# Optimization experiments

Hardware: AMD Instinct MI355X
Metric: run time of the kernel (lower is better)

The kernel has to match this reference:

```python
import jax, jax.numpy as jnp
import numpy as np

CONT_FIELD = 13
CATE_FIELD = 26
VOCAB = 100000
EMB_DIM = 64
HIDDEN = [1024, 1024]
B = 16384
N_FIELDS = CONT_FIELD + CATE_FIELD            # 39
COMB = N_FIELDS * (N_FIELDS - 1) // 2         # 741
FIRST = EMB_DIM * N_FIELDS + COMB             # 3237

# upper-triangular pair indices (i < j), matching the module's rows/cols
_ROWS, _COLS = np.triu_indices(N_FIELDS, k=1)
ROWS = jnp.asarray(_ROWS)
COLS = jnp.asarray(_COLS)


def setup_inputs() -> dict:
    key = jax.random.key(0)
    ks = jax.random.split(key, 12)
    a = np.square(3.0 / (CATE_FIELD * EMB_DIM))
    inp = {
        "conts": jax.random.uniform(ks[0], (B, CONT_FIELD), dtype=jnp.float32),
        "cates": jax.random.randint(ks[1], (B, CATE_FIELD), 0, VOCAB),
        "combs": jax.random.normal(ks[2], (B, COMB), dtype=jnp.float32),
        "emb_table": jax.random.uniform(ks[3], (VOCAB, EMB_DIM), minval=-a, maxval=a, dtype=jnp.float32),
        "W1": jax.random.normal(ks[4], (FIRST, HIDDEN[0]), dtype=jnp.float32) * (6.0 / (FIRST + HIDDEN[0])) ** 0.5,
        "b1": jnp.zeros((HIDDEN[0],), jnp.float32),
        "ln1_g": jnp.ones((HIDDEN[0],), jnp.float32),
        "ln1_b": jnp.zeros((HIDDEN[0],), jnp.float32),
        "W2": jax.random.normal(ks[5], (HIDDEN[0], HIDDEN[1]), dtype=jnp.float32) * (6.0 / (HIDDEN[0] + HIDDEN[1])) ** 0.5,
        "b2": jnp.zeros((HIDDEN[1],), jnp.float32),
        "ln2_g": jnp.ones((HIDDEN[1],), jnp.float32),
        "ln2_b": jnp.zeros((HIDDEN[1],), jnp.float32),
        "Wout": jax.random.normal(ks[6], (HIDDEN[1], 1), dtype=jnp.float32) * (6.0 / (HIDDEN[1] + 1)) ** 0.5,
        "bout": jnp.zeros((1,), jnp.float32),
    }
    return inp


def _layernorm(x, g, b, eps=1e-5):
    mu = jnp.mean(x, axis=-1, keepdims=True)
    var = jnp.mean((x - mu) ** 2, axis=-1, keepdims=True)
    return (x - mu) * jax.lax.rsqrt(var + eps) * g + b


def reference(conts, cates, combs, emb_table, W1, b1, ln1_g, ln1_b,
              W2, b2, ln2_g, ln2_b, Wout, bout):
    # continuous-field embeddings: rows 0..CONT_FIELD-1 of the table, scaled by values
    cont_emb = emb_table[:CONT_FIELD][None, :, :] * conts[:, :, None]   # [B, 13, D]
    cate_emb = emb_table[cates]                                          # [B, 26, D]
    cc = jnp.concatenate([cont_emb, cate_emb], axis=1)                   # [B, 39, D]
    # pairwise inner products: full Gram then upper-triangle extraction
    gram = jnp.einsum("bfd,bgd->bfg", cc, cc)                            # [B, 39, 39]
    pairs = gram[:, ROWS, COLS]                                          # [B, 741]
    X = jnp.concatenate([cont_emb.reshape(cc.shape[0], -1),
                         cate_emb.reshape(cc.shape[0], -1),
                         pairs], axis=1)                                  # [B, 3237]
    X = jax.nn.relu(_layernorm(X @ W1 + b1, ln1_g, ln1_b))
    X = jax.nn.relu(_layernorm(X @ W2 + b2, ln2_g, ln2_b))
    logit = jax.nn.sigmoid(X @ Wout + bout)                               # [B, 1]
    return logit
```

## Files before the change

### kernel.cpp

```cpp
#include <hip/hip_runtime.h>
#include <hip/hip_bf16.h>

#define BATCH 16384
#define NH 1024
#define NF 39
#define CCLD 72
#define KX 2432
#define NPAIR 741
#define FEAT_BLOCKS (BATCH / 4)
#define WPREP_BX (KX / 32 + NH / 32)
#define WPREP_BLOCKS (WPREP_BX * (NH / 32))

typedef __attribute__((ext_vector_type(8))) short bf16x8;
typedef __attribute__((ext_vector_type(4))) float f32x4;

typedef const __attribute__((address_space(1))) unsigned int* gptr_t;
typedef __attribute__((address_space(3))) unsigned int* lptr_t;

__device__ __forceinline__ float bf2f(unsigned short u) {
  union { unsigned int i; float f; } c; c.i = ((unsigned int)u) << 16; return c.f;
}
__device__ __forceinline__ unsigned short f2bf(float f) {
  union { float f; unsigned int i; } c; c.f = f;
  unsigned int r = c.i + 0x7FFFu + ((c.i >> 16) & 1u);
  return (unsigned short)(r >> 16);
}

__global__ __launch_bounds__(256) void prep_kernel(
    const float* __restrict__ conts, const int* __restrict__ cates,
    const float* __restrict__ emb, unsigned short* __restrict__ X,
    const float* __restrict__ W1, const float* __restrict__ W2,
    unsigned short* __restrict__ W1t, unsigned short* __restrict__ W2t) {
  __shared__ __align__(16) unsigned char smem[33664];

  if (blockIdx.x >= FEAT_BLOCKS) {
    int wq = blockIdx.x - FEAT_BLOCKS;
    int bx = wq % WPREP_BX;
    int nb = (wq / WPREP_BX) * 32;
    float (*tile)[33] = (float(*)[33])smem;
    int tx = threadIdx.x & 31, ty = threadIdx.x >> 5;
    if (bx < KX / 32) {
      int kb = bx * 32;
#pragma unroll
      for (int i = 0; i < 32; i += 8) {
        int k = kb + ty + i;
        float v = 0.f;
        if (k < 13) {
          float s = 0.f;
#pragma unroll 8
          for (int d = 0; d < 64; ++d)
            s += emb[k * 64 + d] * W1[(size_t)(k * 64 + d) * NH + nb + tx];
          v = s;
        } else if (k >= 16 && k < 1680) {
          v = W1[(size_t)(832 + k - 16) * NH + nb + tx];
        } else if (k >= 1680 && k < 1680 + NPAIR) {
          v = W1[(size_t)(2496 + k - 1680) * NH + nb + tx];
        }
        tile[ty + i][tx] = v;
      }
      __syncthreads();
#pragma unroll
      for (int i = 0; i < 32; i += 8)
        W1t[(size_t)(nb + ty + i) * KX + kb + tx] = f2bf(tile[tx][ty + i]);
    } else {
      int kb = (bx - KX / 32) * 32;
#pragma unroll
      for (int i = 0; i < 32; i += 8)
        tile[ty + i][tx] = W2[(size_t)(kb + ty + i) * NH + nb + tx];
      __syncthreads();
#pragma unroll
      for (int i = 0; i < 32; i += 8)
        W2t[(size_t)(nb + ty + i) * NH + kb + tx] = f2bf(tile[tx][ty + i]);
    }
    return;
  }

  int wid = threadIdx.x >> 6, lane = threadIdx.x & 63;
  int b = (blockIdx.x << 2) | wid;
  unsigned short* my = (unsigned short*)smem + wid * (48 * CCLD);
  unsigned short* pw = (unsigned short*)(smem + 27648) + wid * 752;
  unsigned short* Xrow = X + (size_t)b * KX;

  int2 c2[13];
#pragma unroll
  for (int i = 0; i < 13; ++i)
    c2[i] = ((const int2*)(cates + b * 26))[i];
  float cf[13];
#pragma unroll
  for (int f = 0; f < 13; ++f) cf[f] = conts[b * 13 + f];
  float cemb[13];
#pragma unroll
  for (int f = 0; f < 13; ++f) cemb[f] = emb[f * 64 + lane];
  float g[26];
#pragma unroll
  for (int j = 0; j < 26; ++j) {
    int idx = (j & 1) ? c2[j >> 1].y : c2[j >> 1].x;
    g[j] = emb[(size_t)idx * 64 + lane];
  }
#pragma unroll
  for (int f = 0; f < 13; ++f)
    my[f * CCLD + lane] = f2bf(cemb[f] * cf[f]);
#pragma unroll
  for (int j = 0; j < 26; ++j)
    my[(13 + j) * CCLD + lane] = f2bf(g[j]);
#pragma unroll
  for (int f = NF; f < 48; ++f) my[f * CCLD + lane] = 0;
  if (lane < 16) Xrow[lane] = (lane < 13) ? f2bf(cf[lane]) : 0;
  if (lane < 752 - NPAIR) pw[NPAIR + lane] = 0;
  __syncthreads();

#pragma unroll
  for (int i = 0; i < 4; ++i) {
    int q = i * 64 + lane;
    if (q < 208)
      *(bf16x8*)&Xrow[16 + q * 8] =
          *(const bf16x8*)&my[(13 + (q >> 3)) * CCLD + (q & 7) * 8];
  }

  int r15 = lane & 15, hi = lane >> 4;
  bf16x8 fr[2][3];
#pragma unroll
  for (int t = 0; t < 3; ++t)
#pragma unroll
    for (int h = 0; h < 2; ++h)
      fr[h][t] = *(const bf16x8*)&my[(t * 16 + r15) * CCLD + h * 32 + hi * 8];

  f32x4 acc[3][3];
#pragma unroll
  for (int it = 0; it < 3; ++it)
#pragma unroll
    for (int jt = 0; jt < 3; ++jt)
      acc[it][jt] = (f32x4){0.f, 0.f, 0.f, 0.f};
#pragma unroll
  for (int h = 0; h < 2; ++h)
#pragma unroll
    for (int it = 0; it < 3; ++it)
#pragma unroll
      for (int jt = 0; jt < 3; ++jt)
        acc[it][jt] = __builtin_amdgcn_mfma_f32_16x16x32_bf16(
            fr[h][it], fr[h][jt], acc[it][jt], 0, 0, 0);

#pragma unroll
  for (int it = 0; it < 3; ++it)
#pragma unroll
    for (int jt = 0; jt < 3; ++jt) {
      int g_ = jt * 16 + r15;
#pragma unroll
      for (int r = 0; r < 4; ++r) {
        int f = it * 16 + hi * 4 + r;
        if (f < g_ && g_ < NF) {
          int p = f * 38 - ((f * (f - 1)) >> 1) + g_ - f - 1;
          pw[p] = f2bf(acc[it][jt][r]);
        }
      }
    }
  __syncthreads();

#pragma unroll
  for (int i = 0; i < 2; ++i) {
    int q = i * 64 + lane;
    if (q < 94)
      *(bf16x8*)&Xrow[1680 + q * 8] = *(const bf16x8*)&pw[q * 8];
  }
}

#define GLL(s_, d_) __builtin_amdgcn_global_load_lds((gptr_t)(s_), (lptr_t)(d_), 16, 0, 0)
#define RD(p_) (*(const bf16x8*)(p_))
#define DSTA(buf, h) (lds + (buf) * 32768 + (h) * 8192 + sd)
#define DSTB(buf, h) (lds + (buf) * 32768 + 16384 + (h) * 8192 + sd)
#define STG(dst, srcb, tau) do { \
    const unsigned short* _s = (srcb) + (size_t)(tau) * 64; \
    GLL(_s, dst); GLL(_s + (size_t)64 * K, (dst) + 4096); } while (0)
#define FENCE() __builtin_amdgcn_sched_barrier(0)
#define MQ(I0, J0, AB, BB) do { \
    _Pragma("unroll") \
    for (int i_ = 0; i_ < 4; ++i_) \
      _Pragma("unroll") \
      for (int j_ = 0; j_ < 2; ++j_) { \
        acc[(I0) + i_][(J0) + j_] = __builtin_amdgcn_mfma_f32_16x16x32_bf16( \
            AB[i_][0], BB[j_][0], acc[(I0) + i_][(J0) + j_], 0, 0, 0); \
        acc[(I0) + i_][(J0) + j_] = __builtin_amdgcn_mfma_f32_16x16x32_bf16( \
            AB[i_][1], BB[j_][1], acc[(I0) + i_][(J0) + j_], 0, 0, 0); \
      } } while (0)

__global__ __launch_bounds__(512, 2) void gemm_8ph(
    const unsigned short* __restrict__ A, const unsigned short* __restrict__ Bt,
    const float* __restrict__ bias, unsigned short* __restrict__ Hout,
    int K, int NT) {
  __shared__ unsigned short lds[65536];

  int bid = blockIdx.x;
  int swz = (bid & 7) * 32 + (bid >> 3);
  int mb = swz >> 2, nb = swz & 3;
  size_t m0 = (size_t)mb * 256, n0 = (size_t)nb * 256;

  int tid = threadIdx.x, lane = tid & 63, w = tid >> 6;
  int wr = w >> 2, wc = w & 3;
  int r15 = lane & 15, hi = lane >> 4;

  int sr = tid >> 3;
  int ce = ((tid & 7) ^ (sr & 7)) << 3;
  int sd = tid * 8;
  const unsigned short* A0p = A + (m0 + sr) * (size_t)K + ce;
  const unsigned short* A1p = A0p + (size_t)128 * K;
  const unsigned short* B0p = Bt + (n0 + sr) * (size_t)K + ce;
  const unsigned short* B1p = B0p + (size_t)128 * K;

  int cbs = (((hi << 4) ^ ((r15 & 7) << 4)) >> 1);
  int rb0 = r15 * 64 + cbs;
  int rb1 = rb0 ^ 32;
  const unsigned short* aH = lds + wr * 8192;
  const unsigned short* bH = lds + 16384 + (wc >> 1) * 8192 + (wc & 1) * 4096;

  f32x4 acc[8][4];
#pragma unroll
  for (int m = 0; m < 8; ++m)
#pragma unroll
    for (int n = 0; n < 4; ++n) acc[m][n] = (f32x4){0.f, 0.f, 0.f, 0.f};

  bf16x8 a0[4][2], a1[4][2], bS[2][2], bR[2][2];

  {
    int t1 = (NT > 1) ? 1 : 0;
    STG(DSTA(0, 0), A0p, 0);
    STG(DSTA(0, 1), A1p, 0);
    STG(DSTB(0, 0), B0p, 0);
    STG(DSTB(0, 1), B1p, 0);
    STG(DSTA(1, 0), A0p, t1);
    STG(DSTA(1, 1), A1p, t1);
    STG(DSTB(1, 0), B0p, t1);
    STG(DSTB(1, 1), B1p, t1);
    asm volatile("s_waitcnt vmcnt(8)" ::: "memory");
    asm volatile("s_barrier" ::: "memory");
    FENCE();
#pragma unroll
    for (int i = 0; i < 4; ++i) {
      a0[i][0] = RD(aH + i * 1024 + rb0);
      a0[i][1] = RD(aH + i * 1024 + rb1);
    }
  }

  for (int t = 0; t < NT; ++t) {
    int cur = t & 1, nxt = cur ^ 1;
    int tc = (t + 2 < NT) ? t + 2 : NT - 1;
    const unsigned short* aBc = aH + cur * 32768;
    const unsigned short* aBn = aH + nxt * 32768;
    const unsigned short* bB = bH + cur * 32768;

#pragma unroll
    for (int j = 0; j < 2; ++j) {
      bS[j][0] = RD(bB + j * 1024 + rb0);
      bS[j][1] = RD(bB + j * 1024 + rb1);
    }
    asm volatile("s_waitcnt lgkmcnt(0)" ::: "memory");
    FENCE();
    __builtin_amdgcn_s_setprio(1);
    MQ(0, 0, a0, bS);
    __builtin_amdgcn_s_setprio(0);
    FENCE();

#pragma unroll
    for (int j = 0; j < 2; ++j) {
      bR[j][0] = RD(bB + (2 + j) * 1024 + rb0);
      bR[j][1] = RD(bB + (2 + j) * 1024 + rb1);
    }
#pragma unroll
    for (int i = 0; i < 4; ++i) {
      a1[i][0] = RD(aBc + (4 + i) * 1024 + rb0);
      a1[i][1] = RD(aBc + (4 + i) * 1024 + rb1);
    }
    asm volatile("s_waitcnt lgkmcnt(8)" ::: "memory");
    FENCE();
    __builtin_amdgcn_s_setprio(1);
    MQ(0, 2, a0, bR);
    __builtin_amdgcn_s_setprio(0);
    asm volatile("s_waitcnt lgkmcnt(0)" ::: "memory");
    asm volatile("s_barrier" ::: "memory");
    FENCE();

    STG(DSTB(cur, 0), B0p, tc);
    STG(DSTA(cur, 0), A0p, tc);
    STG(DSTA(cur, 1), A1p, tc);
    __builtin_amdgcn_s_setprio(1);
    MQ(4, 2, a1, bR);
    __builtin_amdgcn_s_setprio(0);
    FENCE();

    STG(DSTB(cur, 1), B1p, tc);
    asm volatile("s_waitcnt vmcnt(8)" ::: "memory");
    asm volatile("s_barrier" ::: "memory");
    FENCE();
#pragma unroll
    for (int i = 0; i < 4; ++i) {
      a0[i][0] = RD(aBn + i * 1024 + rb0);
      a0[i][1] = RD(aBn + i * 1024 + rb1);
    }
    FENCE();
    __builtin_amdgcn_s_setprio(1);
    MQ(4, 0, a1, bS);
    __builtin_amdgcn_s_setprio(0);
    FENCE();
  }

  size_t crow = m0 + (size_t)wr * 128 + hi * 4;
  size_t ccol = n0 + (size_t)wc * 64 + r15;
  unsigned short* Hp = Hout + crow * NH + ccol;
  float bv[4];
#pragma unroll
  for (int n = 0; n < 4; ++n) bv[n] = bias[ccol + n * 16];
#pragma unroll
  for (int m = 0; m < 8; ++m)
#pragma unroll
    for (int n = 0; n < 4; ++n)
#pragma unroll
      for (int q = 0; q < 4; ++q)
        Hp[(size_t)(m * 16 + q) * NH + n * 16] = f2bf(acc[m][n][q] + bv[n]);
}

__global__ __launch_bounds__(256) void ln_relu_kernel(
    const unsigned short* __restrict__ Yb, const float* __restrict__ gamma,
    const float* __restrict__ beta, unsigned short* __restrict__ H) {
  int wid = threadIdx.x >> 6, lane = threadIdx.x & 63;
  int b = (blockIdx.x << 2) | wid;
  const unsigned short* yrow = Yb + (size_t)b * NH + lane * 16;
  bf16x8 u0 = *(const bf16x8*)&yrow[0];
  bf16x8 u1 = *(const bf16x8*)&yrow[8];
  float v[16];
#pragma unroll
  for (int i = 0; i < 8; ++i) {
    v[i] = bf2f((unsigned short)u0[i]);
    v[8 + i] = bf2f((unsigned short)u1[i]);
  }
  float s1 = 0.f, s2 = 0.f;
#pragma unroll
  for (int i = 0; i < 16; ++i) { s1 += v[i]; s2 += v[i] * v[i]; }
#pragma unroll
  for (int i = 1; i < 64; i <<= 1) {
    s1 += __shfl_xor(s1, i);
    s2 += __shfl_xor(s2, i);
  }
  float mu = s1 * (1.0f / NH);
  float var = s2 * (1.0f / NH) - mu * mu;
  float rs = rsqrtf(var + 1e-5f);
  const float4* gp = (const float4*)(gamma + lane * 16);
  const float4* bp = (const float4*)(beta + lane * 16);
  unsigned short o[16];
#pragma unroll
  for (int q = 0; q < 4; ++q) {
    float4 gg = gp[q], be = bp[q];
    o[q * 4 + 0] = f2bf(fmaxf((v[q * 4 + 0] - mu) * rs * gg.x + be.x, 0.f));
    o[q * 4 + 1] = f2bf(fmaxf((v[q * 4 + 1] - mu) * rs * gg.y + be.y, 0.f));
    o[q * 4 + 2] = f2bf(fmaxf((v[q * 4 + 2] - mu) * rs * gg.z + be.z, 0.f));
    o[q * 4 + 3] = f2bf(fmaxf((v[q * 4 + 3] - mu) * rs * gg.w + be.w, 0.f));
  }
  unsigned short* hrow = H + (size_t)b * NH + lane * 16;
  *(ulonglong2*)&hrow[0] = *(const ulonglong2*)&o[0];
  *(ulonglong2*)&hrow[8] = *(const ulonglong2*)&o[8];
}

__global__ __launch_bounds__(256) void ln_out_kernel(
    const unsigned short* __restrict__ Yb, const float* __restrict__ gamma,
    const float* __restrict__ beta, const float* __restrict__ Wout,
    const float* __restrict__ bout, float* __restrict__ out) {
  int wid = threadIdx.x >> 6, lane = threadIdx.x & 63;
  int b = (blockIdx.x << 2) | wid;
  const unsigned short* yrow = Yb + (size_t)b * NH + lane * 16;
  bf16x8 u0 = *(const bf16x8*)&yrow[0];
  bf16x8 u1 = *(const bf16x8*)&yrow[8];
  float v[16];
#pragma unroll
  for (int i = 0; i < 8; ++i) {
    v[i] = bf2f((unsigned short)u0[i]);
    v[8 + i] = bf2f((unsigned short)u1[i]);
  }
  float s1 = 0.f, s2 = 0.f;
#pragma unroll
  for (int i = 0; i < 16; ++i) { s1 += v[i]; s2 += v[i] * v[i]; }
#pragma unroll
  for (int i = 1; i < 64; i <<= 1) {
    s1 += __shfl_xor(s1, i);
    s2 += __shfl_xor(s2, i);
  }
  float mu = s1 * (1.0f / NH);
  float var = s2 * (1.0f / NH) - mu * mu;
  float rs = rsqrtf(var + 1e-5f);
  const float4* gp = (const float4*)(gamma + lane * 16);
  const float4* bp = (const float4*)(beta + lane * 16);
  const float4* wp = (const float4*)(Wout + lane * 16);
  float s = 0.f;
#pragma unroll
  for (int q = 0; q < 4; ++q) {
    float4 gg = gp[q], be = bp[q], wo = wp[q];
    s += fmaxf((v[q * 4 + 0] - mu) * rs * gg.x + be.x, 0.f) * wo.x;
    s += fmaxf((v[q * 4 + 1] - mu) * rs * gg.y + be.y, 0.f) * wo.y;
    s += fmaxf((v[q * 4 + 2] - mu) * rs * gg.z + be.z, 0.f) * wo.z;
    s += fmaxf((v[q * 4 + 3] - mu) * rs * gg.w + be.w, 0.f) * wo.w;
  }
#pragma unroll
  for (int i = 1; i < 64; i <<= 1) s += __shfl_xor(s, i);
  if (lane == 0) out[b] = 1.f / (1.f + expf(-(s + bout[0])));
}

extern "C" void kernel_launch(void* const* d_in, const int* in_sizes, int n_in,
                              void* d_out, int out_size, void* d_ws, size_t ws_size,
                              hipStream_t stream) {
  const float* conts = (const float*)d_in[0];
  const int* cates = (const int*)d_in[1];
  const float* emb  = (const float*)d_in[3];
  const float* W1   = (const float*)d_in[4];
  const float* b1   = (const float*)d_in[5];
  const float* ln1g = (const float*)d_in[6];
  const float* ln1b = (const float*)d_in[7];
  const float* W2   = (const float*)d_in[8];
  const float* b2   = (const float*)d_in[9];
  const float* ln2g = (const float*)d_in[10];
  const float* ln2b = (const float*)d_in[11];
  const float* Wout = (const float*)d_in[12];
  const float* bout = (const float*)d_in[13];
  float* out = (float*)d_out;

  unsigned short* X   = (unsigned short*)d_ws;
  unsigned short* W1t = X + (size_t)BATCH * KX;
  unsigned short* W2t = W1t + (size_t)NH * KX;
  unsigned short* H1  = W2t + (size_t)NH * NH;
  unsigned short* Yb1 = H1 + (size_t)BATCH * NH;
  unsigned short* Yb2 = Yb1 + (size_t)BATCH * NH;

  hipLaunchKernelGGL(prep_kernel, dim3(FEAT_BLOCKS + WPREP_BLOCKS), dim3(256), 0, stream,
                     conts, cates, emb, X, W1, W2, W1t, W2t);
  hipLaunchKernelGGL(gemm_8ph, dim3(256), dim3(512), 0, stream,
                     X, W1t, b1, Yb1, KX, KX / 64);
  hipLaunchKernelGGL(ln_relu_kernel, dim3(BATCH / 4), dim3(256), 0, stream,
                     Yb1, ln1g, ln1b, H1);
  hipLaunchKernelGGL(gemm_8ph, dim3(256), dim3(512), 0, stream,
                     H1, W2t, b2, Yb2, NH, NH / 64);
  hipLaunchKernelGGL(ln_out_kernel, dim3(BATCH / 4), dim3(256), 0, stream,
                     Yb2, ln2g, ln2b, Wout, bout, out);
}
```

Measured before the change: 168.6 us.

## Restructure GEMM main loop into fine-grained LDS-read/MFMA interleaving by k-half

Reorganizes the per-tile inner loop so that fragments are read from LDS one row-fragment at a time and each 4-MFMA group waits only on its own fragment. The loop walks the two k-halves in order, and the previous register double-buffering of A across iterations is removed. All global-to-LDS staging for the next tile is now issued together before the final two MFMA groups. The aim is tighter overlap of LDS reads with MFMA issue and fewer live fragment registers. The cost is that the first MFMA of each tile now waits on fresh LDS reads after the barrier, and there are more waitcnt points.

After: 175.5 us. 4.1% more time.

```diff
diff --git a/kernel.cpp b/kernel.cpp
--- a/kernel.cpp
+++ b/kernel.cpp
@@ -172,16 +172,20 @@
     const unsigned short* _s = (srcb) + (size_t)(tau) * 64; \
     GLL(_s, dst); GLL(_s + (size_t)64 * K, (dst) + 4096); } while (0)
 #define FENCE() __builtin_amdgcn_sched_barrier(0)
-#define MQ(I0, J0, AB, BB) do { \
+#define RA(M, H) af[M] = RD(aB + (M) * 1024 + ((H) ? rb1 : rb0))
+#define RB(N, H) bf[N][H] = RD(bB + (N) * 1024 + ((H) ? rb1 : rb0))
+#define G4(M, H) do { \
     _Pragma("unroll") \
-    for (int i_ = 0; i_ < 4; ++i_) \
-      _Pragma("unroll") \
-      for (int j_ = 0; j_ < 2; ++j_) { \
-        acc[(I0) + i_][(J0) + j_] = __builtin_amdgcn_mfma_f32_16x16x32_bf16( \
-            AB[i_][0], BB[j_][0], acc[(I0) + i_][(J0) + j_], 0, 0, 0); \
-        acc[(I0) + i_][(J0) + j_] = __builtin_amdgcn_mfma_f32_16x16x32_bf16( \
-            AB[i_][1], BB[j_][1], acc[(I0) + i_][(J0) + j_], 0, 0, 0); \
-      } } while (0)
+    for (int n_ = 0; n_ < 4; ++n_) \
+      acc[M][n_] = __builtin_amdgcn_mfma_f32_16x16x32_bf16( \
+          af[M], bf[n_][H], acc[M][n_], 0, 0, 0); } while (0)
+#define GRP(WAITN, M, H) do { \
+    asm volatile("s_waitcnt lgkmcnt(" #WAITN ")" ::: "memory"); \
+    FENCE(); \
+    __builtin_amdgcn_s_setprio(1); \
+    G4(M, H); \
+    __builtin_amdgcn_s_setprio(0); \
+    FENCE(); } while (0)
 
 __global__ __launch_bounds__(512, 2) void gemm_8ph(
     const unsigned short* __restrict__ A, const unsigned short* __restrict__ Bt,
@@ -218,7 +222,7 @@
 #pragma unroll
     for (int n = 0; n < 4; ++n) acc[m][n] = (f32x4){0.f, 0.f, 0.f, 0.f};
 
-  bf16x8 a0[4][2], a1[4][2], bS[2][2], bR[2][2];
+  bf16x8 af[8], bf[4][2];
 
   {
     int t1 = (NT > 1) ? 1 : 0;
@@ -233,72 +237,45 @@
     asm volatile("s_waitcnt vmcnt(8)" ::: "memory");
     asm volatile("s_barrier" ::: "memory");
     FENCE();
-#pragma unroll
-    for (int i = 0; i < 4; ++i) {
-      a0[i][0] = RD(aH + i * 1024 + rb0);
-      a0[i][1] = RD(aH + i * 1024 + rb1);
-    }
   }
 
   for (int t = 0; t < NT; ++t) {
-    int cur = t & 1, nxt = cur ^ 1;
+    int cur = t & 1;
     int tc = (t + 2 < NT) ? t + 2 : NT - 1;
-    const unsigned short* aBc = aH + cur * 32768;
-    const unsigned short* aBn = aH + nxt * 32768;
+    const unsigned short* aB = aH + cur * 32768;
     const unsigned short* bB = bH + cur * 32768;
 
-#pragma unroll
-    for (int j = 0; j < 2; ++j) {
-      bS[j][0] = RD(bB + j * 1024 + rb0);
-      bS[j][1] = RD(bB + j * 1024 + rb1);
-    }
-    asm volatile("s_waitcnt lgkmcnt(0)" ::: "memory");
-    FENCE();
-    __builtin_amdgcn_s_setprio(1);
-    MQ(0, 0, a0, bS);
-    __builtin_amdgcn_s_setprio(0);
-    FENCE();
-
-#pragma unroll
-    for (int j = 0; j < 2; ++j) {
-      bR[j][0] = RD(bB + (2 + j) * 1024 + rb0);
-      bR[j][1] = RD(bB + (2 + j) * 1024 + rb1);
-    }
-#pragma unroll
-    for (int i = 0; i < 4; ++i) {
-      a1[i][0] = RD(aBc + (4 + i) * 1024 + rb0);
-      a1[i][1] = RD(aBc + (4 + i) * 1024 + rb1);
-    }
-    asm volatile("s_waitcnt lgkmcnt(8)" ::: "memory");
-    FENCE();
-    __builtin_amdgcn_s_setprio(1);
-    MQ(0, 2, a0, bR);
-    __builtin_amdgcn_s_setprio(0);
+    RB(0, 0); RB(1, 0); RB(2, 0); RB(3, 0); RA(0, 0); RA(1, 0); RA(2, 0);
+    GRP(2, 0, 0);
+    RA(3, 0); GRP(2, 1, 0);
+    RA(4, 0); GRP(2, 2, 0);
+    RA(5, 0); GRP(2, 3, 0);
+    RA(6, 0); GRP(2, 4, 0);
+    RA(7, 0); GRP(2, 5, 0);
+    RB(0, 1); RB(1, 1); RB(2, 1); RB(3, 1); RA(0, 1);
+    GRP(6, 6, 0);
+    RA(1, 1); GRP(6, 7, 0);
+    RA(2, 1); GRP(2, 0, 1);
+    RA(3, 1); GRP(2, 1, 1);
+    RA(4, 1); GRP(2, 2, 1);
+    RA(5, 1); GRP(2, 3, 1);
+    RA(6, 1); GRP(2, 4, 1);
+    RA(7, 1); GRP(2, 5, 1);
     asm volatile("s_waitcnt lgkmcnt(0)" ::: "memory");
     asm volatile("s_barrier" ::: "memory");
     FENCE();
 
-    STG(DSTB(cur, 0), B0p, tc);
     STG(DSTA(cur, 0), A0p, tc);
     STG(DSTA(cur, 1), A1p, tc);
+    STG(DSTB(cur, 0), B0p, tc);
+    STG(DSTB(cur, 1), B1p, tc);
     __builtin_amdgcn_s_setprio(1);
-    MQ(4, 2, a1, bR);
+    G4(6, 1);
+    G4(7, 1);
     __builtin_amdgcn_s_setprio(0);
     FENCE();
-
-    STG(DSTB(cur, 1), B1p, tc);
     asm volatile("s_waitcnt vmcnt(8)" ::: "memory");
     asm volatile("s_barrier" ::: "memory");
-    FENCE();
-#pragma unroll
-    for (int i = 0; i < 4; ++i) {
-      a0[i][0] = RD(aBn + i * 1024 + rb0);
-      a0[i][1] = RD(aBn + i * 1024 + rb1);
-    }
-    FENCE();
-    __builtin_amdgcn_s_setprio(1);
-    MQ(4, 0, a1, bS);
-    __builtin_amdgcn_s_setprio(0);
     FENCE();
   }
 
```
